# Kernel optimization log

Measured on AMD Instinct MI355X. Metric: run time of the kernel, lower is better.

The kernel has to match this reference:

```python
import jax, jax.numpy as jnp
import numpy as np

B, CIN, COUT, H, W_SP = 16, 128, 128, 56, 56
E, KH, KW = 4, 3, 3

def setup_inputs() -> dict:
    key = jax.random.key(0)
    k1, k2, k3 = jax.random.split(key, 3)
    x = jax.random.normal(k1, (B, CIN, H, W_SP), dtype=jnp.float32)
    routing_weights = jax.random.uniform(k2, (B, E), dtype=jnp.float32)
    # expert conv kernels, OIHW, stacked over experts: [E, COUT, CIN, KH, KW]
    W = jax.random.normal(k3, (E, COUT, CIN, KH, KW), dtype=jnp.float32) * 0.05
    return {"x": x, "routing_weights": routing_weights, "W": W}

def reference(x, routing_weights, W):
    # Each expert: full Conv2d(stride=1, padding=1, dilation=1, groups=1, no bias)
    def one_expert(w):  # w: [COUT, CIN, KH, KW]
        return jax.lax.conv_general_dilated(
            x, w,
            window_strides=(1, 1),
            padding=((1, 1), (1, 1)),
            dimension_numbers=("NCHW", "OIHW", "NCHW"),
        )
    expert_outs = jax.vmap(one_expert)(W)  # [E, B, COUT, H, W]
    # per-sample scalar mix: sum_e routing[b, e] * expert_outs[e, b]
    out = jnp.einsum("ebchw,be->bchw", expert_outs, routing_weights)
    return out
```

## Files before the change

kernel.cpp:

```cpp
#include <hip/hip_runtime.h>


typedef float  f32x16 __attribute__((ext_vector_type(16)));
typedef short  s16x8  __attribute__((ext_vector_type(8)));
typedef unsigned short u16;

#define CIN   128
#define COUT  128
#define HH    56
#define WW    56
#define SP    (HH*WW)
#define EW    147456
#define BW_   147456
#define XB    16896
#define AB    8192

static __device__ __forceinline__ u16 f2bf(float f) {
    unsigned u = __builtin_bit_cast(unsigned, f);
    return (u16)((u + 0x7FFFu + ((u >> 16) & 1u)) >> 16);
}

static __device__ __forceinline__ void gload16(const void* g, void* l) {
    __builtin_amdgcn_global_load_lds(
        (const __attribute__((address_space(1))) void*)g,
        (__attribute__((address_space(3))) void*)l, 16, 0, 0);
}

__global__ __launch_bounds__(256) void mix_kernel(const float* __restrict__ W,
                                                  const float* __restrict__ r,
                                                  u16* __restrict__ Wmix) {
    int o = blockIdx.x * 256 + threadIdx.x;
    int ci_l = o & 31;
    int o2   = o >> 5;
    int co   = o2 & 127;
    int o3   = o2 >> 7;
    int tap  = o3 % 9;
    int cc   = o3 / 9;
    size_t src = ((size_t)co * CIN + cc*32 + ci_l) * 9 + tap;
    float w0 = W[src], w1 = W[src + EW], w2 = W[src + 2*EW], w3 = W[src + 3*EW];
    #pragma unroll
    for (int b = 0; b < 16; ++b) {
        float acc = r[b*4+0]*w0 + r[b*4+1]*w1 + r[b*4+2]*w2 + r[b*4+3]*w3;
        Wmix[(size_t)b * BW_ + o] = f2bf(acc);
    }
}

__global__ __launch_bounds__(256, 3) void conv_mfma(const float* __restrict__ x,
                                                    const u16* __restrict__ Wmix,
                                                    float* __restrict__ out) {
    __shared__ __align__(16) char ldsb[XB + 4*AB];

    const int bid = blockIdx.x;
    const int bs  = (bid & 7) * 56 + (bid >> 3);
    const int b   = bs / 28;
    const int ph  = bs % 28;
    const int t    = threadIdx.x;
    const int lane = t & 63;
    const int wid  = t >> 6;
    const int wm   = wid >> 1;
    const int wn   = wid & 1;
    const int l31  = lane & 31;
    const int khalf= lane >> 5;

    const u16*   WmixB = Wmix + (size_t)b * BW_;
    const float* xbB   = x + (size_t)b * CIN * SP;

    const int arow = t >> 2;
    const int ssl  = (t & 3) ^ ((t >> 3) & 3);

    f32x16 acc[2][2];
    #pragma unroll
    for (int mf = 0; mf < 2; ++mf)
        #pragma unroll
        for (int nf = 0; nf < 2; ++nf) acc[mf][nf] = (f32x16)0.f;

    auto stageA = [&](int it) {
        char* bufo = ldsb + XB + (it & 3) * AB;
        const u16* ga = WmixB + it * 4096 + arow * 32 + ssl * 8;
        gload16(ga,        bufo + wid * 1024);
        gload16(ga + 2048, bufo + 4096 + wid * 1024);
    };

    auto stageX = [&](int cc) {
        #pragma unroll
        for (int i = 0; i < 4; ++i) {
            int slot = i * 256 + t;
            int c    = 1 + (slot & 63);
            int row  = (slot >> 6) & 3;
            int g    = slot >> 8;
            int rr   = 2*ph - 1 + row;
            int w    = c - 1;
            const float* p = xbB + (size_t)(cc*32 + g*8) * SP + rr*56 + w;
            bool rowok = (unsigned)rr < 56u;
            bool colok = w < 56;
            s16x8 v;
            #pragma unroll
            for (int j = 0; j < 8; ++j) {
                float f = (rowok && colok) ? p[j * SP] : 0.f;
                v[j] = (short)f2bf(f);
            }
            int so = ((row*66 + c)*64) + ((g ^ ((c >> 1) & 3)) * 16);
            *(s16x8*)(ldsb + so) = v;
        }
    };

    auto compute = [&](int it, int kh, int kw) {
        const char* Ab = ldsb + XB + (it & 3) * AB;
        #pragma unroll
        for (int ksub = 0; ksub < 2; ++ksub) {
            const int s = ksub * 2 + khalf;
            s16x8 af[2], bv[2];
            #pragma unroll
            for (int mf = 0; mf < 2; ++mf)
                af[mf] = *(const s16x8*)(Ab + (wm*64 + mf*32 + l31)*64
                                            + ((s ^ ((l31 >> 1) & 3)) * 16));
            #pragma unroll
            for (int nf = 0; nf < 2; ++nf) {
                const int c = l31 + nf*32 + kw;
                bv[nf] = *(const s16x8*)(ldsb + ((wn + kh)*66 + c)*64
                                              + ((s ^ ((c >> 1) & 3)) * 16));
            }
            #pragma unroll
            for (int mf = 0; mf < 2; ++mf)
                #pragma unroll
                for (int nf = 0; nf < 2; ++nf)
                    acc[mf][nf] = __builtin_amdgcn_mfma_f32_32x32x16_bf16(
                        af[mf], bv[nf], acc[mf][nf], 0, 0, 0);
        }
    };

    if (t < 32) {
        int row = t >> 3, ch = ((t >> 2) & 1) ? 65 : 0, sl = t & 3;
        *(s16x8*)(ldsb + (row*66 + ch)*64 + sl*16) = (s16x8)0;
    }
    stageX(0);
    stageA(0);
    stageA(1);
    asm volatile("s_waitcnt lgkmcnt(0)" ::: "memory");

    #pragma unroll
    for (int cc = 0; cc < 4; ++cc) {
        if (cc) {
            __builtin_amdgcn_s_barrier();
            stageX(cc);
            asm volatile("s_waitcnt lgkmcnt(0)" ::: "memory");
            __builtin_amdgcn_sched_barrier(0);
        }
        #pragma unroll
        for (int tap = 0; tap < 9; ++tap) {
            const int it = cc * 9 + tap;
            if (it + 2 < 36) {
                stageA(it + 2);
                asm volatile("s_waitcnt vmcnt(4)" ::: "memory");
            } else if (it + 1 < 36) {
                asm volatile("s_waitcnt vmcnt(2)" ::: "memory");
            } else {
                asm volatile("s_waitcnt vmcnt(0)" ::: "memory");
            }
            __builtin_amdgcn_s_barrier();
            __builtin_amdgcn_sched_barrier(0);
            __builtin_amdgcn_s_setprio(1);
            compute(it, tap / 3, tap % 3);
            __builtin_amdgcn_s_setprio(0);
            __builtin_amdgcn_sched_barrier(0);
        }
    }

    #pragma unroll
    for (int nf = 0; nf < 2; ++nf) {
        const int w = nf * 32 + l31;
        if (w < 56) {
            const int hrow = 2 * ph + wn;
            #pragma unroll
            for (int mf = 0; mf < 2; ++mf) {
                #pragma unroll
                for (int rg = 0; rg < 16; ++rg) {
                    int co = wm*64 + mf*32 + (rg & 3) + 8*(rg >> 2) + 4*khalf;
                    out[(((size_t)b*COUT + co)*HH + hrow)*WW + w] = acc[mf][nf][rg];
                }
            }
        }
    }
}

extern "C" void kernel_launch(void* const* d_in, const int* in_sizes, int n_in,
                              void* d_out, int out_size, void* d_ws, size_t ws_size,
                              hipStream_t stream) {
    const float* x = (const float*)d_in[0];
    const float* r = (const float*)d_in[1];
    const float* W = (const float*)d_in[2];
    float* outp = (float*)d_out;
    u16* Wmix = (u16*)d_ws;

    mix_kernel<<<576, 256, 0, stream>>>(W, r, Wmix);
    conv_mfma <<<448, 256, 0, stream>>>(x, Wmix, outp);
}
```

Measured before the change: 36.81 us.

## Load mixed weights straight to registers and drop LDS staging of A

The weight (A) operand no longer goes through LDS via global_load_lds. Each wave now loads its A fragments directly from global memory into a three-deep register ring, prefetching two iterations ahead. This removes the per-tap workgroup barrier and the vmcnt waits tied to LDS staging. The x tile switches from an XOR-swizzled layout to a padded row stride of 72 bytes, and staging is simplified to one column per thread, with an extra barrier after each x restage. The trade-off is more VGPR pressure under a 3-blocks-per-CU bound, and global latency is exposed directly to the MFMAs, with no explicit waits and reliance on compiler-inserted vmcnt.

```diff
diff --git a/kernel.cpp b/kernel.cpp
--- a/kernel.cpp
+++ b/kernel.cpp
@@ -12,18 +12,11 @@
 #define SP    (HH*WW)
 #define EW    147456
 #define BW_   147456
-#define XB    16896
-#define AB    8192
+#define XSTR  72
 
 static __device__ __forceinline__ u16 f2bf(float f) {
     unsigned u = __builtin_bit_cast(unsigned, f);
     return (u16)((u + 0x7FFFu + ((u >> 16) & 1u)) >> 16);
-}
-
-static __device__ __forceinline__ void gload16(const void* g, void* l) {
-    __builtin_amdgcn_global_load_lds(
-        (const __attribute__((address_space(1))) void*)g,
-        (__attribute__((address_space(3))) void*)l, 16, 0, 0);
 }
 
 __global__ __launch_bounds__(256) void mix_kernel(const float* __restrict__ W,
@@ -48,7 +41,7 @@
 __global__ __launch_bounds__(256, 3) void conv_mfma(const float* __restrict__ x,
                                                     const u16* __restrict__ Wmix,
                                                     float* __restrict__ out) {
-    __shared__ __align__(16) char ldsb[XB + 4*AB];
+    __shared__ __align__(16) char ldsb[4 * 66 * XSTR];
 
     const int bid = blockIdx.x;
     const int bs  = (bid & 7) * 56 + (bid >> 3);
@@ -65,106 +58,100 @@
     const u16*   WmixB = Wmix + (size_t)b * BW_;
     const float* xbB   = x + (size_t)b * CIN * SP;
 
-    const int arow = t >> 2;
-    const int ssl  = (t & 3) ^ ((t >> 3) & 3);
-
     f32x16 acc[2][2];
     #pragma unroll
     for (int mf = 0; mf < 2; ++mf)
         #pragma unroll
         for (int nf = 0; nf < 2; ++nf) acc[mf][nf] = (f32x16)0.f;
 
-    auto stageA = [&](int it) {
-        char* bufo = ldsb + XB + (it & 3) * AB;
-        const u16* ga = WmixB + it * 4096 + arow * 32 + ssl * 8;
-        gload16(ga,        bufo + wid * 1024);
-        gload16(ga + 2048, bufo + 4096 + wid * 1024);
-    };
+    const int sc   = 1 + (t & 63);
+    const int srow = t >> 6;
+    const int srr  = 2*ph - 1 + srow;
+    const int sw   = sc - 1;
+    const bool sok = ((unsigned)srr < 56u) && (sw < 56);
+    const float* sp = xbB + (size_t)srr * 56 + sw;
+    char* sdst = ldsb + (srow*66 + sc) * XSTR;
 
     auto stageX = [&](int cc) {
         #pragma unroll
         for (int i = 0; i < 4; ++i) {
-            int slot = i * 256 + t;
-            int c    = 1 + (slot & 63);
-            int row  = (slot >> 6) & 3;
-            int g    = slot >> 8;
-            int rr   = 2*ph - 1 + row;
-            int w    = c - 1;
-            const float* p = xbB + (size_t)(cc*32 + g*8) * SP + rr*56 + w;
-            bool rowok = (unsigned)rr < 56u;
-            bool colok = w < 56;
             s16x8 v;
             #pragma unroll
             for (int j = 0; j < 8; ++j) {
-                float f = (rowok && colok) ? p[j * SP] : 0.f;
+                float f = sok ? sp[(size_t)(cc*32 + i*8 + j) * SP] : 0.f;
                 v[j] = (short)f2bf(f);
             }
-            int so = ((row*66 + c)*64) + ((g ^ ((c >> 1) & 3)) * 16);
-            *(s16x8*)(ldsb + so) = v;
+            *(s16x8*)(sdst + i*16) = v;
         }
     };
 
-    auto compute = [&](int it, int kh, int kw) {
-        const char* Ab = ldsb + XB + (it & 3) * AB;
-        #pragma unroll
-        for (int ksub = 0; ksub < 2; ++ksub) {
-            const int s = ksub * 2 + khalf;
-            s16x8 af[2], bv[2];
-            #pragma unroll
-            for (int mf = 0; mf < 2; ++mf)
-                af[mf] = *(const s16x8*)(Ab + (wm*64 + mf*32 + l31)*64
-                                            + ((s ^ ((l31 >> 1) & 3)) * 16));
-            #pragma unroll
-            for (int nf = 0; nf < 2; ++nf) {
-                const int c = l31 + nf*32 + kw;
-                bv[nf] = *(const s16x8*)(ldsb + ((wn + kh)*66 + c)*64
-                                              + ((s ^ ((c >> 1) & 3)) * 16));
-            }
-            #pragma unroll
-            for (int mf = 0; mf < 2; ++mf)
-                #pragma unroll
-                for (int nf = 0; nf < 2; ++nf)
-                    acc[mf][nf] = __builtin_amdgcn_mfma_f32_32x32x16_bf16(
-                        af[mf], bv[nf], acc[mf][nf], 0, 0, 0);
-        }
-    };
+    const u16* abase = WmixB + (wm*64 + l31)*32 + khalf*8;
+    s16x8 aset[3][4];
+#define ALOAD(IT, S) {                                             \
+    const u16* ap_ = abase + (IT)*4096;                            \
+    aset[S][0] = *(const s16x8*)(ap_);              \
+    aset[S][1] = *(const s16x8*)(ap_ + 16);         \
+    aset[S][2] = *(const s16x8*)(ap_ + 1024);       \
+    aset[S][3] = *(const s16x8*)(ap_ + 1040); }
 
     if (t < 32) {
-        int row = t >> 3, ch = ((t >> 2) & 1) ? 65 : 0, sl = t & 3;
-        *(s16x8*)(ldsb + (row*66 + ch)*64 + sl*16) = (s16x8)0;
+        int row = t >> 3, col = ((t >> 2) & 1) ? 65 : 0, sl = t & 3;
+        *(s16x8*)(ldsb + (row*66 + col)*XSTR + sl*16) = (s16x8)0;
     }
+    ALOAD(0, 0)
+    ALOAD(1, 1)
     stageX(0);
-    stageA(0);
-    stageA(1);
     asm volatile("s_waitcnt lgkmcnt(0)" ::: "memory");
+    __builtin_amdgcn_sched_barrier(0);
+    __builtin_amdgcn_s_barrier();
+    __builtin_amdgcn_sched_barrier(0);
 
     #pragma unroll
     for (int cc = 0; cc < 4; ++cc) {
         if (cc) {
+            __builtin_amdgcn_sched_barrier(0);
             __builtin_amdgcn_s_barrier();
+            __builtin_amdgcn_sched_barrier(0);
             stageX(cc);
             asm volatile("s_waitcnt lgkmcnt(0)" ::: "memory");
+            __builtin_amdgcn_sched_barrier(0);
+            __builtin_amdgcn_s_barrier();
             __builtin_amdgcn_sched_barrier(0);
         }
         #pragma unroll
         for (int tap = 0; tap < 9; ++tap) {
             const int it = cc * 9 + tap;
+            const int kh = tap / 3;
+            const int kw = tap % 3;
             if (it + 2 < 36) {
-                stageA(it + 2);
-                asm volatile("s_waitcnt vmcnt(4)" ::: "memory");
-            } else if (it + 1 < 36) {
-                asm volatile("s_waitcnt vmcnt(2)" ::: "memory");
-            } else {
-                asm volatile("s_waitcnt vmcnt(0)" ::: "memory");
+                switch ((it + 2) % 3) {
+                    case 0: ALOAD(it + 2, 0) break;
+                    case 1: ALOAD(it + 2, 1) break;
+                    case 2: ALOAD(it + 2, 2) break;
+                }
             }
-            __builtin_amdgcn_s_barrier();
             __builtin_amdgcn_sched_barrier(0);
             __builtin_amdgcn_s_setprio(1);
-            compute(it, tap / 3, tap % 3);
+            #pragma unroll
+            for (int ksub = 0; ksub < 2; ++ksub) {
+                const int s = ksub * 2 + khalf;
+                s16x8 bv[2];
+                #pragma unroll
+                for (int nf = 0; nf < 2; ++nf) {
+                    const int c = l31 + nf*32 + kw;
+                    bv[nf] = *(const s16x8*)(ldsb + ((wn + kh)*66 + c)*XSTR + s*16);
+                }
+                #pragma unroll
+                for (int mf = 0; mf < 2; ++mf)
+                    #pragma unroll
+                    for (int nf = 0; nf < 2; ++nf)
+                        acc[mf][nf] = __builtin_amdgcn_mfma_f32_32x32x16_bf16(
+                            aset[it % 3][mf*2 + ksub], bv[nf], acc[mf][nf], 0, 0, 0);
+            }
             __builtin_amdgcn_s_setprio(0);
-            __builtin_amdgcn_sched_barrier(0);
         }
     }
+#undef ALOAD
 
     #pragma unroll
     for (int nf = 0; nf < 2; ++nf) {
```

Measured after the change: 41.46 us. 1.13x slower.

## Split conv tile across 8 waves and pad X tile stride instead of swizzle

Applied to the files above, without the earlier changes.

Doubles the block to 512 threads so each of 8 waves computes one 64-wide column half, with half the accumulators per wave. Each thread now issues one weight global_load_lds and two X staging slots instead of two and four, and the vmcnt waits are adjusted to match. The X tile in LDS switches from an XOR swizzle to a padded 72-byte row stride to avoid bank conflicts. An extra barrier after X staging is added. The aim is more waves to hide latency and lower register pressure per thread, at the cost of more barrier traffic and a larger LDS footprint per block.

```diff
diff --git a/kernel.cpp b/kernel.cpp
--- a/kernel.cpp
+++ b/kernel.cpp
@@ -12,7 +12,8 @@
 #define SP    (HH*WW)
 #define EW    147456
 #define BW_   147456
-#define XB    16896
+#define XSTR  72
+#define XB    (4*66*XSTR)
 #define AB    8192
 
 static __device__ __forceinline__ u16 f2bf(float f) {
@@ -45,7 +46,7 @@
     }
 }
 
-__global__ __launch_bounds__(256, 3) void conv_mfma(const float* __restrict__ x,
+__global__ __launch_bounds__(512, 4) void conv_mfma(const float* __restrict__ x,
                                                     const u16* __restrict__ Wmix,
                                                     float* __restrict__ out) {
     __shared__ __align__(16) char ldsb[XB + 4*AB];
@@ -57,50 +58,45 @@
     const int t    = threadIdx.x;
     const int lane = t & 63;
     const int wid  = t >> 6;
-    const int wm   = wid >> 1;
-    const int wn   = wid & 1;
+    const int wm   = (wid >> 2) & 1;
+    const int wn   = (wid >> 1) & 1;
+    const int wp   = wid & 1;
     const int l31  = lane & 31;
     const int khalf= lane >> 5;
 
     const u16*   WmixB = Wmix + (size_t)b * BW_;
     const float* xbB   = x + (size_t)b * CIN * SP;
 
-    const int arow = t >> 2;
-    const int ssl  = (t & 3) ^ ((t >> 3) & 3);
+    const int ssl = (t & 3) ^ ((t >> 3) & 3);
 
-    f32x16 acc[2][2];
-    #pragma unroll
-    for (int mf = 0; mf < 2; ++mf)
-        #pragma unroll
-        for (int nf = 0; nf < 2; ++nf) acc[mf][nf] = (f32x16)0.f;
+    f32x16 acc[2];
+    acc[0] = (f32x16)0.f;
+    acc[1] = (f32x16)0.f;
 
     auto stageA = [&](int it) {
-        char* bufo = ldsb + XB + (it & 3) * AB;
-        const u16* ga = WmixB + it * 4096 + arow * 32 + ssl * 8;
-        gload16(ga,        bufo + wid * 1024);
-        gload16(ga + 2048, bufo + 4096 + wid * 1024);
+        char* ldst = ldsb + XB + (it & 3) * AB + wid * 1024;
+        const u16* ga = WmixB + it * 4096 + (t >> 2) * 32 + ssl * 8;
+        gload16(ga, ldst);
     };
 
     auto stageX = [&](int cc) {
         #pragma unroll
-        for (int i = 0; i < 4; ++i) {
-            int slot = i * 256 + t;
+        for (int i = 0; i < 2; ++i) {
+            int slot = i * 512 + t;
             int c    = 1 + (slot & 63);
             int row  = (slot >> 6) & 3;
             int g    = slot >> 8;
             int rr   = 2*ph - 1 + row;
             int w    = c - 1;
+            bool ok  = ((unsigned)rr < 56u) && (w < 56);
             const float* p = xbB + (size_t)(cc*32 + g*8) * SP + rr*56 + w;
-            bool rowok = (unsigned)rr < 56u;
-            bool colok = w < 56;
             s16x8 v;
             #pragma unroll
             for (int j = 0; j < 8; ++j) {
-                float f = (rowok && colok) ? p[j * SP] : 0.f;
+                float f = ok ? p[(size_t)j * SP] : 0.f;
                 v[j] = (short)f2bf(f);
             }
-            int so = ((row*66 + c)*64) + ((g ^ ((c >> 1) & 3)) * 16);
-            *(s16x8*)(ldsb + so) = v;
+            *(s16x8*)(ldsb + (row*66 + c)*XSTR + g*16) = v;
         }
     };
 
@@ -109,41 +105,42 @@
         #pragma unroll
         for (int ksub = 0; ksub < 2; ++ksub) {
             const int s = ksub * 2 + khalf;
-            s16x8 af[2], bv[2];
+            s16x8 af[2], bv;
             #pragma unroll
             for (int mf = 0; mf < 2; ++mf)
                 af[mf] = *(const s16x8*)(Ab + (wm*64 + mf*32 + l31)*64
                                             + ((s ^ ((l31 >> 1) & 3)) * 16));
-            #pragma unroll
-            for (int nf = 0; nf < 2; ++nf) {
-                const int c = l31 + nf*32 + kw;
-                bv[nf] = *(const s16x8*)(ldsb + ((wn + kh)*66 + c)*64
-                                              + ((s ^ ((c >> 1) & 3)) * 16));
-            }
+            const int c = wp*32 + l31 + kw;
+            bv = *(const s16x8*)(ldsb + ((wn + kh)*66 + c)*XSTR + s*16);
             #pragma unroll
             for (int mf = 0; mf < 2; ++mf)
-                #pragma unroll
-                for (int nf = 0; nf < 2; ++nf)
-                    acc[mf][nf] = __builtin_amdgcn_mfma_f32_32x32x16_bf16(
-                        af[mf], bv[nf], acc[mf][nf], 0, 0, 0);
+                acc[mf] = __builtin_amdgcn_mfma_f32_32x32x16_bf16(
+                    af[mf], bv, acc[mf], 0, 0, 0);
         }
     };
 
     if (t < 32) {
-        int row = t >> 3, ch = ((t >> 2) & 1) ? 65 : 0, sl = t & 3;
-        *(s16x8*)(ldsb + (row*66 + ch)*64 + sl*16) = (s16x8)0;
+        int row = t >> 3, col = ((t >> 2) & 1) ? 65 : 0, sl = t & 3;
+        *(s16x8*)(ldsb + (row*66 + col)*XSTR + sl*16) = (s16x8)0;
     }
-    stageX(0);
     stageA(0);
     stageA(1);
+    stageX(0);
     asm volatile("s_waitcnt lgkmcnt(0)" ::: "memory");
+    __builtin_amdgcn_sched_barrier(0);
+    __builtin_amdgcn_s_barrier();
+    __builtin_amdgcn_sched_barrier(0);
 
     #pragma unroll
     for (int cc = 0; cc < 4; ++cc) {
         if (cc) {
+            __builtin_amdgcn_sched_barrier(0);
             __builtin_amdgcn_s_barrier();
+            __builtin_amdgcn_sched_barrier(0);
             stageX(cc);
             asm volatile("s_waitcnt lgkmcnt(0)" ::: "memory");
+            __builtin_amdgcn_sched_barrier(0);
+            __builtin_amdgcn_s_barrier();
             __builtin_amdgcn_sched_barrier(0);
         }
         #pragma unroll
@@ -151,9 +148,9 @@
             const int it = cc * 9 + tap;
             if (it + 2 < 36) {
                 stageA(it + 2);
-                asm volatile("s_waitcnt vmcnt(4)" ::: "memory");
+                asm volatile("s_waitcnt vmcnt(2)" ::: "memory");
             } else if (it + 1 < 36) {
-                asm volatile("s_waitcnt vmcnt(2)" ::: "memory");
+                asm volatile("s_waitcnt vmcnt(1)" ::: "memory");
             } else {
                 asm volatile("s_waitcnt vmcnt(0)" ::: "memory");
             }
@@ -162,22 +159,18 @@
             __builtin_amdgcn_s_setprio(1);
             compute(it, tap / 3, tap % 3);
             __builtin_amdgcn_s_setprio(0);
-            __builtin_amdgcn_sched_barrier(0);
         }
     }
 
-    #pragma unroll
-    for (int nf = 0; nf < 2; ++nf) {
-        const int w = nf * 32 + l31;
-        if (w < 56) {
-            const int hrow = 2 * ph + wn;
+    const int w = wp * 32 + l31;
+    if (w < 56) {
+        const int hrow = 2 * ph + wn;
+        #pragma unroll
+        for (int mf = 0; mf < 2; ++mf) {
             #pragma unroll
-            for (int mf = 0; mf < 2; ++mf) {
-                #pragma unroll
-                for (int rg = 0; rg < 16; ++rg) {
-                    int co = wm*64 + mf*32 + (rg & 3) + 8*(rg >> 2) + 4*khalf;
-                    out[(((size_t)b*COUT + co)*HH + hrow)*WW + w] = acc[mf][nf][rg];
-                }
+            for (int rg = 0; rg < 16; ++rg) {
+                int co = wm*64 + mf*32 + (rg & 3) + 8*(rg >> 2) + 4*khalf;
+                out[(((size_t)b*COUT + co)*HH + hrow)*WW + w] = acc[mf][rg];
             }
         }
     }
@@ -193,5 +186,5 @@
     u16* Wmix = (u16*)d_ws;
 
     mix_kernel<<<576, 256, 0, stream>>>(W, r, Wmix);
-    conv_mfma <<<448, 256, 0, stream>>>(x, Wmix, outp);
+    conv_mfma <<<448, 512, 0, stream>>>(x, Wmix, outp);
 }
```

New measurement: 34.47 us. 6.4% less time.
